# Kernel optimization log

Measured on AMD Instinct MI355X. Metric: run time of the kernel, lower is better.

Reference implementation:

```python
import jax, jax.numpy as jnp
import numpy as np
import math

IN_F = 256
OUT_F = 256
HEADS = 4
HEAD_DIM = OUT_F // HEADS
B, N = 4, 2048


def setup_inputs() -> dict:
    key = jax.random.key(0)
    ks = jax.random.split(key, 7)
    s = 1.0 / math.sqrt(IN_F)
    h = jax.random.normal(ks[0], (B, N, IN_F), dtype=jnp.float32)
    adj = jax.random.randint(ks[1], (N, N), 0, 2, dtype=jnp.int32)
    Wq = jax.random.uniform(ks[2], (IN_F, OUT_F), jnp.float32, -s, s)
    Wk = jax.random.uniform(ks[3], (IN_F, OUT_F), jnp.float32, -s, s)
    Wv = jax.random.uniform(ks[4], (IN_F, OUT_F), jnp.float32, -s, s)
    Wo = jax.random.uniform(ks[5], (OUT_F, OUT_F), jnp.float32, -s, s)
    bo = jax.random.uniform(ks[6], (OUT_F,), jnp.float32, -s, s)
    return {"h": h, "adj": adj, "Wq": Wq, "Wk": Wk, "Wv": Wv, "Wo": Wo, "bo": bo}


def reference(h, adj, Wq, Wk, Wv, Wo, bo):
    Bv, Nv, _ = h.shape
    # project and split heads: [B, H, N, Dh]
    q = (h @ Wq).reshape(Bv, Nv, HEADS, HEAD_DIM).transpose(0, 2, 1, 3)
    k = (h @ Wk).reshape(Bv, Nv, HEADS, HEAD_DIM).transpose(0, 2, 1, 3)
    v = (h @ Wv).reshape(Bv, Nv, HEADS, HEAD_DIM).transpose(0, 2, 1, 3)
    scores = jnp.einsum('bhnd,bhmd->bhnm', q, k) / math.sqrt(HEAD_DIM)
    mask = (adj == 0)[None, None, :, :]  # [1,1,N,N]
    scores = jnp.where(mask, jnp.float32(-1e9), scores)
    attn = jax.nn.softmax(scores, axis=-1)  # dropout is identity in eval / p=0
    out = jnp.einsum('bhnm,bhmd->bhnd', attn, v)
    out = out.transpose(0, 2, 1, 3).reshape(Bv, Nv, OUT_F)
    return h + out @ Wo + bo
```

## Files before the change

kernel.cpp:

```cpp
#include <hip/hip_runtime.h>
#include <hip/hip_bf16.h>

#define B_ 4
#define N_ 2048
#define F_ 256
#define H_ 4
#define D_ 64

typedef __attribute__((ext_vector_type(8))) short short8;
typedef __attribute__((ext_vector_type(4))) float f32x4;

__device__ __forceinline__ unsigned short f2bf(float x) {
  unsigned u = __builtin_bit_cast(unsigned, x);
  u = (u + 0x7fffu + ((u >> 16) & 1u)) >> 16;
  return (unsigned short)u;
}

__device__ __forceinline__ float bf2f(unsigned short x) {
  unsigned u = ((unsigned)x) << 16;
  return __builtin_bit_cast(float, u);
}

__device__ __forceinline__ f32x4 mfma16(short8 a, short8 b, f32x4 c) {
  return __builtin_amdgcn_mfma_f32_16x16x32_bf16(a, b, c, 0, 0, 0);
}

#define QSCALE 0.1803368801111204f

__global__ __launch_bounds__(256) void prep_kernel(
    const float* __restrict__ h, const int* __restrict__ adj,
    const float* __restrict__ Wq, const float* __restrict__ Wk,
    const float* __restrict__ Wv, const float* __restrict__ Wo,
    unsigned short* __restrict__ hbf,
    unsigned short* __restrict__ wqt, unsigned short* __restrict__ wkt,
    unsigned short* __restrict__ wvt, unsigned short* __restrict__ wot,
    unsigned* __restrict__ adjp) {
  int bid = blockIdx.x;
  int tid = threadIdx.x;
  if (bid < 2048) {
    int idx = (bid * 256 + tid) * 4;
    float4 v = *(const float4*)(h + idx);
    ushort4 o;
    o.x = f2bf(v.x); o.y = f2bf(v.y); o.z = f2bf(v.z); o.w = f2bf(v.w);
    *(ushort4*)(hbf + idx) = o;
  } else if (bid < 3072) {
    int t = (bid - 2048) * 256 + tid;
    int w = t >> 16;
    int e = t & 65535;
    int i = e >> 8;
    int o = e & 255;
    const float* W = (w == 0) ? Wq : (w == 1) ? Wk : (w == 2) ? Wv : Wo;
    unsigned short* Wt = (w == 0) ? wqt : (w == 1) ? wkt : (w == 2) ? wvt : wot;
    Wt[o * 256 + i] = f2bf(W[i * 256 + o]);
  } else {
    int lane = tid & 63;
    int wid = (bid - 3072) * 4 + (tid >> 6);
    unsigned long long* adjp64 = (unsigned long long*)adjp;
    #pragma unroll
    for (int it = 0; it < 16; ++it) {
      int widx = wid * 16 + it;
      int base = widx * 64 + lane;
      unsigned long long m = __ballot(adj[base] != 0);
      if (lane == 0) adjp64[widx] = m;
    }
  }
}

__global__ __launch_bounds__(256) void qkv_gemm(
    const unsigned short* __restrict__ hbf,
    const unsigned short* __restrict__ wqt, const unsigned short* __restrict__ wkt,
    const unsigned short* __restrict__ wvt,
    unsigned short* __restrict__ qb, unsigned short* __restrict__ kb,
    unsigned short* __restrict__ vtb) {
  int lane = threadIdx.x & 63;
  int wv = threadIdx.x >> 6;
  int g = lane >> 4;
  int c = lane & 15;
  int row64 = blockIdx.x * 256 + wv * 64;
  int colbase = blockIdx.y * 64;
  int which = colbase >> 8;
  int fbase = colbase & 255;
  const unsigned short* wt = (which == 0) ? wqt : (which == 1) ? wkt : wvt;

  f32x4 acc[4][4];
  #pragma unroll
  for (int rt = 0; rt < 4; ++rt)
    #pragma unroll
    for (int cc = 0; cc < 4; ++cc) acc[rt][cc] = (f32x4){0.f, 0.f, 0.f, 0.f};

  for (int k = 0; k < 256; k += 32) {
    short8 a[4], b[4];
    #pragma unroll
    for (int rt = 0; rt < 4; ++rt)
      a[rt] = *(const short8*)(hbf + (row64 + rt * 16 + c) * 256 + k + g * 8);
    #pragma unroll
    for (int cc = 0; cc < 4; ++cc)
      b[cc] = *(const short8*)(wt + (fbase + cc * 16 + c) * 256 + k + g * 8);
    #pragma unroll
    for (int rt = 0; rt < 4; ++rt)
      #pragma unroll
      for (int cc = 0; cc < 4; ++cc)
        acc[rt][cc] = mfma16(a[rt], b[cc], acc[rt][cc]);
  }

  #pragma unroll
  for (int rt = 0; rt < 4; ++rt) {
    #pragma unroll
    for (int cc = 0; cc < 4; ++cc) {
      #pragma unroll
      for (int r = 0; r < 4; ++r) {
        int row = row64 + rt * 16 + g * 4 + r;
        int f = fbase + cc * 16 + c;
        int hh = f >> 6, d = f & 63;
        int bb = row >> 11, n = row & 2047;
        float v = acc[rt][cc][r];
        if (which == 0)
          qb[((bb * H_ + hh) * N_ + n) * D_ + d] = f2bf(v * QSCALE);
        else if (which == 1)
          kb[((bb * H_ + hh) * N_ + n) * D_ + d] = f2bf(v);
        else
          vtb[((bb * H_ + hh) * D_ + d) * N_ + n] = f2bf(v);
      }
    }
  }
}

__global__ __launch_bounds__(256) void attn_kernel(
    const unsigned short* __restrict__ qb, const unsigned short* __restrict__ kb,
    const unsigned short* __restrict__ vtb, const unsigned* __restrict__ adjp,
    unsigned short* __restrict__ Opart, float* __restrict__ Lp) {
  __shared__ __align__(16) unsigned short plds[4][32 * 40];
  int lane = threadIdx.x & 63;
  int wv = threadIdx.x >> 6;
  int g = lane >> 4;
  int c = lane & 15;
  int task = blockIdx.x * 4 + wv;
  int s = task & 3;
  int qt = (task >> 2) & 63;
  int bh = task >> 8;
  int qbase = qt * 32;
  const unsigned short* Qp = qb + bh * (N_ * D_);
  const unsigned short* Kp = kb + bh * (N_ * D_);
  const unsigned short* Vt = vtb + bh * (D_ * N_);
  unsigned short* myp = plds[wv];

  short8 qf[2][2];
  #pragma unroll
  for (int rt = 0; rt < 2; ++rt)
    #pragma unroll
    for (int dh = 0; dh < 2; ++dh)
      qf[rt][dh] = *(const short8*)(Qp + (qbase + rt * 16 + c) * D_ + dh * 32 + g * 8);

  f32x4 O[2][4];
  float Lsum[2][4];
  #pragma unroll
  for (int rt = 0; rt < 2; ++rt) {
    #pragma unroll
    for (int dt = 0; dt < 4; ++dt) O[rt][dt] = (f32x4){0.f, 0.f, 0.f, 0.f};
    #pragma unroll
    for (int r = 0; r < 4; ++r) Lsum[rt][r] = 0.f;
  }

  const f32x4 z4 = {0.f, 0.f, 0.f, 0.f};
  int kv0 = s * 512;

  for (int mb = kv0; mb < kv0 + 512; mb += 32) {
    int mw = mb >> 5;
    short8 kf[2][2];
    #pragma unroll
    for (int mt = 0; mt < 2; ++mt)
      #pragma unroll
      for (int dh = 0; dh < 2; ++dh)
        kf[mt][dh] = *(const short8*)(Kp + (mb + mt * 16 + c) * D_ + dh * 32 + g * 8);

    f32x4 S[2][2];
    #pragma unroll
    for (int rt = 0; rt < 2; ++rt)
      #pragma unroll
      for (int mt = 0; mt < 2; ++mt) {
        f32x4 ss = mfma16(qf[rt][0], kf[mt][0], z4);
        S[rt][mt] = mfma16(qf[rt][1], kf[mt][1], ss);
      }

    #pragma unroll
    for (int rt = 0; rt < 2; ++rt) {
      #pragma unroll
      for (int r = 0; r < 4; ++r) {
        int n = qbase + rt * 16 + g * 4 + r;
        unsigned aw = adjp[n * 64 + mw];
        float e0 = __builtin_amdgcn_exp2f(S[rt][0][r]);
        float e1 = __builtin_amdgcn_exp2f(S[rt][1][r]);
        float p0 = ((aw >> c) & 1u) ? e0 : 0.f;
        float p1 = ((aw >> (c + 16)) & 1u) ? e1 : 0.f;
        Lsum[rt][r] += p0 + p1;
        unsigned pr;
        asm("v_cvt_pk_bf16_f32 %0, %1, %2" : "=v"(pr) : "v"(p0), "v"(p1));
        int prow = rt * 16 + g * 4 + r;
        myp[prow * 40 + c] = (unsigned short)pr;
        myp[prow * 40 + 16 + c] = (unsigned short)(pr >> 16);
      }
    }

    short8 pa[2];
    #pragma unroll
    for (int rt = 0; rt < 2; ++rt)
      pa[rt] = *(const short8*)(myp + (rt * 16 + c) * 40 + g * 8);

    #pragma unroll
    for (int dt = 0; dt < 4; ++dt) {
      short8 vf = *(const short8*)(Vt + (dt * 16 + c) * N_ + mb + g * 8);
      #pragma unroll
      for (int rt = 0; rt < 2; ++rt)
        O[rt][dt] = mfma16(pa[rt], vf, O[rt][dt]);
    }
  }

  unsigned short* Ob = Opart + (size_t)task * 2048;
  #pragma unroll
  for (int rt = 0; rt < 2; ++rt) {
    #pragma unroll
    for (int r = 0; r < 4; ++r) {
      float l = Lsum[rt][r];
      l += __shfl_xor(l, 1);
      l += __shfl_xor(l, 2);
      l += __shfl_xor(l, 4);
      l += __shfl_xor(l, 8);
      int row = rt * 16 + g * 4 + r;
      if (c == 0) Lp[task * 32 + row] = l;
      #pragma unroll
      for (int dt = 0; dt < 4; ++dt)
        Ob[row * 64 + dt * 16 + c] = f2bf(O[rt][dt][r]);
    }
  }
}

__global__ __launch_bounds__(256) void combine_kernel(
    const unsigned short* __restrict__ Opart, const float* __restrict__ Lp,
    unsigned short* __restrict__ ao) {
  int t = blockIdx.x * 256 + threadIdx.x;
  int dq = t & 3;
  int n = (t >> 2) & 2047;
  int bh = t >> 13;
  int qt = n >> 5, row32 = n & 31;
  int tbase = bh * 256 + qt * 4;

  float Lg = 0.f;
  #pragma unroll
  for (int s = 0; s < 4; ++s) Lg += Lp[(tbase + s) * 32 + row32];
  float inv = 1.0f / Lg;

  float o[16];
  #pragma unroll
  for (int d = 0; d < 16; ++d) o[d] = 0.f;
  #pragma unroll
  for (int s = 0; s < 4; ++s) {
    const unsigned short* p = Opart + (size_t)(tbase + s) * 2048 + row32 * 64 + dq * 16;
    short8 v0 = *(const short8*)(p);
    short8 v1 = *(const short8*)(p + 8);
    #pragma unroll
    for (int d = 0; d < 8; ++d) {
      o[d]     += bf2f((unsigned short)v0[d]);
      o[8 + d] += bf2f((unsigned short)v1[d]);
    }
  }

  int bb = bh >> 2, hh = bh & 3;
  short8 ob0, ob1;
  #pragma unroll
  for (int d = 0; d < 8; ++d) {
    ob0[d] = (short)f2bf(o[d] * inv);
    ob1[d] = (short)f2bf(o[8 + d] * inv);
  }
  unsigned short* dst = ao + ((size_t)(bb * N_ + n)) * F_ + hh * 64 + dq * 16;
  *(short8*)(dst) = ob0;
  *(short8*)(dst + 8) = ob1;
}

__global__ __launch_bounds__(256) void out_gemm(
    const unsigned short* __restrict__ ao, const unsigned short* __restrict__ wot,
    const float* __restrict__ h, const float* __restrict__ bo,
    float* __restrict__ out) {
  int lane = threadIdx.x & 63;
  int wv = threadIdx.x >> 6;
  int g = lane >> 4;
  int c = lane & 15;
  int row64 = blockIdx.x * 256 + wv * 64;
  int colb = blockIdx.y * 64;

  f32x4 acc[4][4];
  #pragma unroll
  for (int rt = 0; rt < 4; ++rt)
    #pragma unroll
    for (int cc = 0; cc < 4; ++cc) acc[rt][cc] = (f32x4){0.f, 0.f, 0.f, 0.f};

  for (int k = 0; k < 256; k += 32) {
    short8 a[4], b[4];
    #pragma unroll
    for (int rt = 0; rt < 4; ++rt)
      a[rt] = *(const short8*)(ao + (row64 + rt * 16 + c) * 256 + k + g * 8);
    #pragma unroll
    for (int cc = 0; cc < 4; ++cc)
      b[cc] = *(const short8*)(wot + (colb + cc * 16 + c) * 256 + k + g * 8);
    #pragma unroll
    for (int rt = 0; rt < 4; ++rt)
      #pragma unroll
      for (int cc = 0; cc < 4; ++cc)
        acc[rt][cc] = mfma16(a[rt], b[cc], acc[rt][cc]);
  }

  #pragma unroll
  for (int rt = 0; rt < 4; ++rt) {
    #pragma unroll
    for (int cc = 0; cc < 4; ++cc) {
      #pragma unroll
      for (int r = 0; r < 4; ++r) {
        int row = row64 + rt * 16 + g * 4 + r;
        int col = colb + cc * 16 + c;
        out[row * 256 + col] = h[row * 256 + col] + bo[col] + acc[rt][cc][r];
      }
    }
  }
}

extern "C" void kernel_launch(void* const* d_in, const int* in_sizes, int n_in,
                              void* d_out, int out_size, void* d_ws, size_t ws_size,
                              hipStream_t stream) {
  (void)in_sizes; (void)n_in; (void)out_size; (void)ws_size;
  const float* h  = (const float*)d_in[0];
  const int* adj  = (const int*)d_in[1];
  const float* Wq = (const float*)d_in[2];
  const float* Wk = (const float*)d_in[3];
  const float* Wv = (const float*)d_in[4];
  const float* Wo = (const float*)d_in[5];
  const float* bo = (const float*)d_in[6];
  float* out = (float*)d_out;

  char* ws = (char*)d_ws;
  unsigned short* hbf = (unsigned short*)(ws + 0);
  unsigned short* wqt = (unsigned short*)(ws + 4194304);
  unsigned short* wkt = (unsigned short*)(ws + 4325376);
  unsigned short* wvt = (unsigned short*)(ws + 4456448);
  unsigned short* wot = (unsigned short*)(ws + 4587520);
  unsigned*       adjp = (unsigned*)(ws + 4718592);
  unsigned short* qb  = (unsigned short*)(ws + 5242880);
  unsigned short* kb  = (unsigned short*)(ws + 9437184);
  unsigned short* vtb = (unsigned short*)(ws + 13631488);
  unsigned short* ao  = (unsigned short*)(ws + 17825792);
  unsigned short* Opart = (unsigned short*)(ws + 22020096);
  float*          Lp  = (float*)(ws + 38797312);

  prep_kernel<<<4096, 256, 0, stream>>>(h, adj, Wq, Wk, Wv, Wo,
                                        hbf, wqt, wkt, wvt, wot, adjp);
  qkv_gemm<<<dim3(32, 12), 256, 0, stream>>>(hbf, wqt, wkt, wvt, qb, kb, vtb);
  attn_kernel<<<1024, 256, 0, stream>>>(qb, kb, vtb, adjp, Opart, Lp);
  combine_kernel<<<512, 256, 0, stream>>>(Opart, Lp, ao);
  out_gemm<<<dim3(32, 4), 256, 0, stream>>>(ao, wot, h, bo, out);
}
```

Measured before the change: 210.0 us.

## Transpose adjacency bitmask, prefetch K tiles, double-buffer P, and shrink GEMM tiles

The adjacency bitmask is stored transposed (key-word major) so each lane can fetch four query rows' mask words with one vector load instead of eight scalar loads. The attention loop now prefetches the next K tile into registers and double-buffers the per-wave P staging area in LDS. Blocks are remapped so the four waves of a block handle the four KV splits of the same query tile, with blocks interleaved across heads. The QKV and output GEMMs use smaller per-wave row tiles and launch more blocks, trading per-wave reuse for more parallelism on the GPU.

```diff
diff --git a/kernel.cpp b/kernel.cpp
--- a/kernel.cpp
+++ b/kernel.cpp
@@ -9,6 +9,7 @@
 
 typedef __attribute__((ext_vector_type(8))) short short8;
 typedef __attribute__((ext_vector_type(4))) float f32x4;
+typedef __attribute__((ext_vector_type(4))) unsigned u32x4;
 
 __device__ __forceinline__ unsigned short f2bf(float x) {
   unsigned u = __builtin_bit_cast(unsigned, x);
@@ -34,7 +35,7 @@
     unsigned short* __restrict__ hbf,
     unsigned short* __restrict__ wqt, unsigned short* __restrict__ wkt,
     unsigned short* __restrict__ wvt, unsigned short* __restrict__ wot,
-    unsigned* __restrict__ adjp) {
+    unsigned* __restrict__ adjt) {
   int bid = blockIdx.x;
   int tid = threadIdx.x;
   if (bid < 2048) {
@@ -55,13 +56,16 @@
   } else {
     int lane = tid & 63;
     int wid = (bid - 3072) * 4 + (tid >> 6);
-    unsigned long long* adjp64 = (unsigned long long*)adjp;
     #pragma unroll
     for (int it = 0; it < 16; ++it) {
       int widx = wid * 16 + it;
-      int base = widx * 64 + lane;
-      unsigned long long m = __ballot(adj[base] != 0);
-      if (lane == 0) adjp64[widx] = m;
+      int n = widx >> 5;
+      int mw64 = widx & 31;
+      unsigned long long m = __ballot(adj[widx * 64 + lane] != 0);
+      if (lane == 0) {
+        adjt[(2 * mw64) * 2048 + n] = (unsigned)m;
+        adjt[(2 * mw64 + 1) * 2048 + n] = (unsigned)(m >> 32);
+      }
     }
   }
 }
@@ -76,40 +80,40 @@
   int wv = threadIdx.x >> 6;
   int g = lane >> 4;
   int c = lane & 15;
-  int row64 = blockIdx.x * 256 + wv * 64;
+  int row32 = blockIdx.x * 128 + wv * 32;
   int colbase = blockIdx.y * 64;
   int which = colbase >> 8;
   int fbase = colbase & 255;
   const unsigned short* wt = (which == 0) ? wqt : (which == 1) ? wkt : wvt;
 
-  f32x4 acc[4][4];
-  #pragma unroll
-  for (int rt = 0; rt < 4; ++rt)
+  f32x4 acc[2][4];
+  #pragma unroll
+  for (int rt = 0; rt < 2; ++rt)
     #pragma unroll
     for (int cc = 0; cc < 4; ++cc) acc[rt][cc] = (f32x4){0.f, 0.f, 0.f, 0.f};
 
   for (int k = 0; k < 256; k += 32) {
-    short8 a[4], b[4];
-    #pragma unroll
-    for (int rt = 0; rt < 4; ++rt)
-      a[rt] = *(const short8*)(hbf + (row64 + rt * 16 + c) * 256 + k + g * 8);
+    short8 a[2], b[4];
+    #pragma unroll
+    for (int rt = 0; rt < 2; ++rt)
+      a[rt] = *(const short8*)(hbf + (row32 + rt * 16 + c) * 256 + k + g * 8);
     #pragma unroll
     for (int cc = 0; cc < 4; ++cc)
       b[cc] = *(const short8*)(wt + (fbase + cc * 16 + c) * 256 + k + g * 8);
     #pragma unroll
-    for (int rt = 0; rt < 4; ++rt)
+    for (int rt = 0; rt < 2; ++rt)
       #pragma unroll
       for (int cc = 0; cc < 4; ++cc)
         acc[rt][cc] = mfma16(a[rt], b[cc], acc[rt][cc]);
   }
 
   #pragma unroll
-  for (int rt = 0; rt < 4; ++rt) {
+  for (int rt = 0; rt < 2; ++rt) {
     #pragma unroll
     for (int cc = 0; cc < 4; ++cc) {
       #pragma unroll
       for (int r = 0; r < 4; ++r) {
-        int row = row64 + rt * 16 + g * 4 + r;
+        int row = row32 + rt * 16 + g * 4 + r;
         int f = fbase + cc * 16 + c;
         int hh = f >> 6, d = f & 63;
         int bb = row >> 11, n = row & 2047;
@@ -127,22 +131,22 @@
 
 __global__ __launch_bounds__(256) void attn_kernel(
     const unsigned short* __restrict__ qb, const unsigned short* __restrict__ kb,
-    const unsigned short* __restrict__ vtb, const unsigned* __restrict__ adjp,
+    const unsigned short* __restrict__ vtb, const unsigned* __restrict__ adjt,
     unsigned short* __restrict__ Opart, float* __restrict__ Lp) {
-  __shared__ __align__(16) unsigned short plds[4][32 * 40];
+  __shared__ __align__(16) unsigned short plds[4][2][32 * 40];
   int lane = threadIdx.x & 63;
   int wv = threadIdx.x >> 6;
   int g = lane >> 4;
   int c = lane & 15;
-  int task = blockIdx.x * 4 + wv;
-  int s = task & 3;
-  int qt = (task >> 2) & 63;
-  int bh = task >> 8;
+  int lb = (blockIdx.x & 7) * 128 + (blockIdx.x >> 3);
+  int bh = lb >> 6;
+  int qt = lb & 63;
+  int s = wv;
+  int task = bh * 256 + qt * 4 + s;
   int qbase = qt * 32;
   const unsigned short* Qp = qb + bh * (N_ * D_);
   const unsigned short* Kp = kb + bh * (N_ * D_);
   const unsigned short* Vt = vtb + bh * (D_ * N_);
-  unsigned short* myp = plds[wv];
 
   short8 qf[2][2];
   #pragma unroll
@@ -164,30 +168,42 @@
   const f32x4 z4 = {0.f, 0.f, 0.f, 0.f};
   int kv0 = s * 512;
 
-  for (int mb = kv0; mb < kv0 + 512; mb += 32) {
+  short8 kfa[2][2], kfb[2][2];
+  #pragma unroll
+  for (int mt = 0; mt < 2; ++mt)
+    #pragma unroll
+    for (int dh = 0; dh < 2; ++dh)
+      kfa[mt][dh] = *(const short8*)(Kp + (kv0 + mt * 16 + c) * D_ + dh * 32 + g * 8);
+
+  for (int it = 0; it < 16; ++it) {
+    int mb = kv0 + it * 32;
     int mw = mb >> 5;
-    short8 kf[2][2];
+    int nmb = (it == 15) ? kv0 : (mb + 32);
     #pragma unroll
     for (int mt = 0; mt < 2; ++mt)
       #pragma unroll
       for (int dh = 0; dh < 2; ++dh)
-        kf[mt][dh] = *(const short8*)(Kp + (mb + mt * 16 + c) * D_ + dh * 32 + g * 8);
+        kfb[mt][dh] = *(const short8*)(Kp + (nmb + mt * 16 + c) * D_ + dh * 32 + g * 8);
+    u32x4 awq[2];
+    #pragma unroll
+    for (int rt = 0; rt < 2; ++rt)
+      awq[rt] = *(const u32x4*)(adjt + mw * 2048 + qbase + rt * 16 + g * 4);
 
     f32x4 S[2][2];
     #pragma unroll
     for (int rt = 0; rt < 2; ++rt)
       #pragma unroll
       for (int mt = 0; mt < 2; ++mt) {
-        f32x4 ss = mfma16(qf[rt][0], kf[mt][0], z4);
-        S[rt][mt] = mfma16(qf[rt][1], kf[mt][1], ss);
+        f32x4 ss = mfma16(qf[rt][0], kfa[mt][0], z4);
+        S[rt][mt] = mfma16(qf[rt][1], kfa[mt][1], ss);
       }
 
+    unsigned short* myp = plds[wv][it & 1];
     #pragma unroll
     for (int rt = 0; rt < 2; ++rt) {
       #pragma unroll
       for (int r = 0; r < 4; ++r) {
-        int n = qbase + rt * 16 + g * 4 + r;
-        unsigned aw = adjp[n * 64 + mw];
+        unsigned aw = awq[rt][r];
         float e0 = __builtin_amdgcn_exp2f(S[rt][0][r]);
         float e1 = __builtin_amdgcn_exp2f(S[rt][1][r]);
         float p0 = ((aw >> c) & 1u) ? e0 : 0.f;
@@ -213,6 +229,12 @@
       for (int rt = 0; rt < 2; ++rt)
         O[rt][dt] = mfma16(pa[rt], vf, O[rt][dt]);
     }
+
+    #pragma unroll
+    for (int mt = 0; mt < 2; ++mt)
+      #pragma unroll
+      for (int dh = 0; dh < 2; ++dh)
+        kfa[mt][dh] = kfb[mt][dh];
   }
 
   unsigned short* Ob = Opart + (size_t)task * 2048;
@@ -284,40 +306,30 @@
   int wv = threadIdx.x >> 6;
   int g = lane >> 4;
   int c = lane & 15;
-  int row64 = blockIdx.x * 256 + wv * 64;
+  int row16 = blockIdx.x * 64 + wv * 16;
   int colb = blockIdx.y * 64;
-
-  f32x4 acc[4][4];
-  #pragma unroll
-  for (int rt = 0; rt < 4; ++rt)
-    #pragma unroll
-    for (int cc = 0; cc < 4; ++cc) acc[rt][cc] = (f32x4){0.f, 0.f, 0.f, 0.f};
+  int arow = row16 + c;
+
+  f32x4 acc[4];
+  #pragma unroll
+  for (int cc = 0; cc < 4; ++cc) acc[cc] = (f32x4){0.f, 0.f, 0.f, 0.f};
 
   for (int k = 0; k < 256; k += 32) {
-    short8 a[4], b[4];
-    #pragma unroll
-    for (int rt = 0; rt < 4; ++rt)
-      a[rt] = *(const short8*)(ao + (row64 + rt * 16 + c) * 256 + k + g * 8);
-    #pragma unroll
-    for (int cc = 0; cc < 4; ++cc)
-      b[cc] = *(const short8*)(wot + (colb + cc * 16 + c) * 256 + k + g * 8);
-    #pragma unroll
-    for (int rt = 0; rt < 4; ++rt)
-      #pragma unroll
-      for (int cc = 0; cc < 4; ++cc)
-        acc[rt][cc] = mfma16(a[rt], b[cc], acc[rt][cc]);
-  }
-
-  #pragma unroll
-  for (int rt = 0; rt < 4; ++rt) {
+    short8 a = *(const short8*)(ao + arow * 256 + k + g * 8);
     #pragma unroll
     for (int cc = 0; cc < 4; ++cc) {
-      #pragma unroll
-      for (int r = 0; r < 4; ++r) {
-        int row = row64 + rt * 16 + g * 4 + r;
-        int col = colb + cc * 16 + c;
-        out[row * 256 + col] = h[row * 256 + col] + bo[col] + acc[rt][cc][r];
-      }
+      short8 bfrag = *(const short8*)(wot + (colb + cc * 16 + c) * 256 + k + g * 8);
+      acc[cc] = mfma16(a, bfrag, acc[cc]);
+    }
+  }
+
+  #pragma unroll
+  for (int cc = 0; cc < 4; ++cc) {
+    #pragma unroll
+    for (int r = 0; r < 4; ++r) {
+      int row = row16 + g * 4 + r;
+      int col = colb + cc * 16 + c;
+      out[row * 256 + col] = h[row * 256 + col] + bo[col] + acc[cc][r];
     }
   }
 }
@@ -341,7 +353,7 @@
   unsigned short* wkt = (unsigned short*)(ws + 4325376);
   unsigned short* wvt = (unsigned short*)(ws + 4456448);
   unsigned short* wot = (unsigned short*)(ws + 4587520);
-  unsigned*       adjp = (unsigned*)(ws + 4718592);
+  unsigned*       adjt = (unsigned*)(ws + 4718592);
   unsigned short* qb  = (unsigned short*)(ws + 5242880);
   unsigned short* kb  = (unsigned short*)(ws + 9437184);
   unsigned short* vtb = (unsigned short*)(ws + 13631488);
@@ -350,9 +362,9 @@
   float*          Lp  = (float*)(ws + 38797312);
 
   prep_kernel<<<4096, 256, 0, stream>>>(h, adj, Wq, Wk, Wv, Wo,
-                                        hbf, wqt, wkt, wvt, wot, adjp);
-  qkv_gemm<<<dim3(32, 12), 256, 0, stream>>>(hbf, wqt, wkt, wvt, qb, kb, vtb);
-  attn_kernel<<<1024, 256, 0, stream>>>(qb, kb, vtb, adjp, Opart, Lp);
+                                        hbf, wqt, wkt, wvt, wot, adjt);
+  qkv_gemm<<<dim3(64, 12), 256, 0, stream>>>(hbf, wqt, wkt, wvt, qb, kb, vtb);
+  attn_kernel<<<1024, 256, 0, stream>>>(qb, kb, vtb, adjt, Opart, Lp);
   combine_kernel<<<512, 256, 0, stream>>>(Opart, Lp, ao);
-  out_gemm<<<dim3(32, 4), 256, 0, stream>>>(ao, wot, h, bo, out);
-}
+  out_gemm<<<dim3(128, 4), 256, 0, stream>>>(ao, wot, h, bo, out);
+}
```

Result: faster. 199.9 us (-4.8%).
